# Kernel tuning notes

Hardware: AMD Instinct MI355X
Metric: run time of the kernel (lower is better)

The kernel has to match this reference:

```python
import jax, jax.numpy as jnp
import numpy as np
from jax import lax

# ---- Haar (db1) wavelet filters, matching create_wavelet_filter ----
_S2 = float(1.0 / np.sqrt(2.0))
_dec_lo = np.array([_S2, _S2], np.float32)    # pywt dec_lo reversed (symmetric)
_dec_hi = np.array([_S2, -_S2], np.float32)   # pywt dec_hi [-s,s] reversed
_rec_lo = np.array([_S2, _S2], np.float32)    # pywt rec_lo flipped (symmetric)
_rec_hi = np.array([-_S2, _S2], np.float32)   # pywt rec_hi [s,-s] flipped

def _outer(a, b):  # torch: a.unsqueeze(0) * b.unsqueeze(1) -> [i,j] = a[j]*b[i]
    return b[:, None] * a[None, :]

DEC = jnp.asarray(np.stack([_outer(_dec_lo, _dec_lo), _outer(_dec_lo, _dec_hi),
                            _outer(_dec_hi, _dec_lo), _outer(_dec_hi, _dec_hi)]))  # [4,2,2]
REC = jnp.asarray(np.stack([_outer(_rec_lo, _rec_lo), _outer(_rec_lo, _rec_hi),
                            _outer(_rec_hi, _rec_lo), _outer(_rec_hi, _rec_hi)]))  # [4,2,2]

BN_EPS = 1e-5

def mish(x):
    return x * jnp.tanh(jax.nn.softplus(x))

def silu(x):
    return x * jax.nn.sigmoid(x)

def bn(x, g, b):  # eval-mode BatchNorm2d with running_mean=0, running_var=1
    return x * (g / jnp.sqrt(1.0 + BN_EPS))[None, :, None, None] + b[None, :, None, None]

def dwconv(x, w, pad):  # depthwise conv, w: [C,1,k,k]
    return lax.conv_general_dilated(x, w, (1, 1), [(pad, pad), (pad, pad)],
                                    feature_group_count=x.shape[1],
                                    dimension_numbers=('NCHW', 'OIHW', 'NCHW'))

def dyn_dwconv(x, ew, gw):
    # DynamicConv2d (depthwise experts). ew: [E,C,1,k,k], gw: [E,C]
    gates = jax.nn.softmax(x.mean((2, 3)) @ gw.T, axis=-1)  # [B,E]
    k = ew.shape[-1]
    outs = jnp.stack([dwconv(x, ew[e], k // 2) for e in range(ew.shape[0])], 1)  # [B,E,C,H,W]
    return jnp.einsum('be,bechw->bchw', gates, outs)

def local_branch(x, ew, gw, bn1g, bn1b, pw, bn2g, bn2b):
    # DWConv2d_BN_ReLU: dynamic dwconv -> BN -> Mish -> depthwise 1x1 (per-channel scale) -> BN
    y = mish(bn(dyn_dwconv(x, ew, gw), bn1g, bn1b))
    y = y * pw[None, :, None, None]
    return bn(y, bn2g, bn2b)

def sel_scan(u, xw, dtw, dtb, Alog, Dp):
    # u: [B,L,D]; xw: [R+2N,D]; dtw: [D,R]; dtb: [D]; Alog: [D,N]; Dp: [D]
    R = dtw.shape[1]
    N = Alog.shape[1]
    xdbl = jnp.einsum('bld,ed->ble', u, xw)
    dt, Bm, Cm = xdbl[..., :R], xdbl[..., R:R + N], xdbl[..., R + N:]
    delta = jax.nn.softplus(jnp.einsum('blr,dr->bld', dt, dtw) + dtb)  # [B,L,D]
    A = -jnp.exp(Alog)                                                  # [D,N]
    a = jnp.exp(delta[..., None] * A)                                   # [B,L,D,N]
    b = delta[..., None] * Bm[:, :, None, :] * u[..., None]             # [B,L,D,N]
    def comb(c1, c2):
        a1, b1 = c1
        a2, b2 = c2
        return a1 * a2, a2 * b1 + b2
    _, h = lax.associative_scan(comb, (a, b), axis=1)                    # h_t = a_t h_{t-1} + b_t
    return jnp.einsum('bldn,bln->bld', h, Cm) + Dp * u

def ss2d(x, in_w, cw, cb, xpw, dtw, dtb, Alog, Dp, ow):
    # SS2D (d_state=1, k_group=2, channel_first): in_proj -> dwconv+silu -> 2-direction
    # selective scan -> gate with silu(z) -> out_proj.
    B, C, H, W = x.shape
    xz = jnp.einsum('oc,bchw->bohw', in_w, x)
    d = in_w.shape[0] // 2
    xi, z = xz[:, :d], xz[:, d:]
    xc = silu(dwconv(xi, cw, 1) + cb[None, :, None, None])
    u0 = xc.reshape(B, d, H * W).transpose(0, 2, 1)                       # row-major scan
    u1 = xc.transpose(0, 1, 3, 2).reshape(B, d, H * W).transpose(0, 2, 1)  # col-major scan
    y0 = sel_scan(u0, xpw[0], dtw[0], dtb[0], Alog[0], Dp[0])
    y1 = sel_scan(u1, xpw[1], dtw[1], dtb[1], Alog[1], Dp[1])
    y0 = y0.transpose(0, 2, 1).reshape(B, d, H, W)
    y1 = y1.transpose(0, 2, 1).reshape(B, d, W, H).transpose(0, 1, 3, 2)
    y = (y0 + y1) * silu(z)
    return jnp.einsum('oc,bchw->bohw', ow, y)

def mbwt(x, wav_w, wav_b, wav_scale, base_scale,
         ss_in_w, ss_conv_w, ss_conv_b, ss_xproj_w, ss_dt_w, ss_dt_b, ss_A_log, ss_D, ss_out_w):
    # MBWTConv2d, wt_levels=1, H/W even. Haar WT (2x2 stride 2) == block reshape + einsum.
    B, C, H, W = x.shape
    xr = x.reshape(B, C, H // 2, 2, W // 2, 2)
    wt = jnp.einsum('bchpwq,kpq->bckhw', xr, DEC)                  # [B,C,4,h,w]
    tag = wt.reshape(B, 4 * C, H // 2, W // 2)
    tag = dwconv(tag, wav_w, wav_w.shape[-1] // 2) + wav_b[None, :, None, None]
    tag = (tag * wav_scale).reshape(B, C, 4, H // 2, W // 2)
    # inverse Haar WT (conv_transpose 2x2 stride 2, groups=C)
    up = jnp.einsum('bckhw,kpq->bchpwq', tag, REC).reshape(B, C, H, W)
    g = ss2d(x, ss_in_w, ss_conv_w, ss_conv_b, ss_xproj_w, ss_dt_w, ss_dt_b, ss_A_log, ss_D, ss_out_w)
    return base_scale * g + up


def setup_inputs() -> dict:
    key = jax.random.key(0)
    ks = iter(jax.random.split(key, 64))
    B, DIM, H, W = 16, 256, 64, 64
    Cg = Cl = 64
    d = {'x': jax.random.normal(next(ks), (B, DIM, H, W), jnp.float32)}
    for j, k in enumerate((3, 5, 7)):
        p = f'l{j}_'
        d[p + 'ew'] = jax.random.normal(next(ks), (4, Cl, 1, k, k), jnp.float32) * 0.1
        d[p + 'gw'] = jax.random.normal(next(ks), (4, Cl), jnp.float32) * 0.1
        d[p + 'bn1g'] = jnp.ones((Cl,), jnp.float32)
        d[p + 'bn1b'] = jnp.zeros((Cl,), jnp.float32)
        d[p + 'pw'] = jax.random.normal(next(ks), (Cl,), jnp.float32) * 0.2
        d[p + 'bn2g'] = jnp.ones((Cl,), jnp.float32)
        d[p + 'bn2b'] = jnp.zeros((Cl,), jnp.float32)
    d['wav_w'] = jax.random.normal(next(ks), (4 * Cg, 1, 3, 3), jnp.float32) * 0.1
    d['wav_b'] = jnp.zeros((4 * Cg,), jnp.float32)
    d['wav_scale'] = jnp.full((1, 4 * Cg, 1, 1), 0.1, jnp.float32)
    d['base_scale'] = jnp.ones((1, Cg, 1, 1), jnp.float32)
    dm, R, N, K = Cg, 4, 1, 2  # d_inner, dt_rank, d_state, k_group
    d['ss_in_w'] = jax.random.normal(next(ks), (2 * dm, Cg), jnp.float32) * float(1 / np.sqrt(Cg))
    d['ss_conv_w'] = jax.random.normal(next(ks), (dm, 1, 3, 3), jnp.float32) * 0.1
    d['ss_conv_b'] = jnp.zeros((dm,), jnp.float32)
    d['ss_xproj_w'] = jax.random.normal(next(ks), (K, R + 2 * N, dm), jnp.float32) * float(1 / np.sqrt(dm))
    d['ss_dt_w'] = jax.random.normal(next(ks), (K, dm, R), jnp.float32) * float(1 / np.sqrt(R))
    d['ss_dt_b'] = jnp.full((K, dm), -2.0, jnp.float32)
    d['ss_A_log'] = jnp.zeros((K, dm, N), jnp.float32)
    d['ss_D'] = jnp.ones((K, dm), jnp.float32)
    d['ss_out_w'] = jax.random.normal(next(ks), (Cg, dm), jnp.float32) * float(1 / np.sqrt(dm))
    return d


def reference(x,
              l0_ew, l0_gw, l0_bn1g, l0_bn1b, l0_pw, l0_bn2g, l0_bn2b,
              l1_ew, l1_gw, l1_bn1g, l1_bn1b, l1_pw, l1_bn2g, l1_bn2b,
              l2_ew, l2_gw, l2_bn1g, l2_bn1b, l2_pw, l2_bn2g, l2_bn2b,
              wav_w, wav_b, wav_scale, base_scale,
              ss_in_w, ss_conv_w, ss_conv_b, ss_xproj_w, ss_dt_w, ss_dt_b, ss_A_log, ss_D, ss_out_w):
    Cg, Cl = 64, 64
    xg, xl, xi = x[:, :Cg], x[:, Cg:Cg + Cl], x[:, Cg + Cl:]
    yl = (local_branch(xl, l0_ew, l0_gw, l0_bn1g, l0_bn1b, l0_pw, l0_bn2g, l0_bn2b)
          + local_branch(xl, l1_ew, l1_gw, l1_bn1g, l1_bn1b, l1_pw, l1_bn2g, l1_bn2b)
          + local_branch(xl, l2_ew, l2_gw, l2_bn1g, l2_bn1b, l2_pw, l2_bn2g, l2_bn2b))
    yg = mbwt(xg, wav_w, wav_b, wav_scale, base_scale,
              ss_in_w, ss_conv_w, ss_conv_b, ss_xproj_w, ss_dt_w, ss_dt_b, ss_A_log, ss_D, ss_out_w)
    return jnp.concatenate([yg, yl, xi], axis=1)
```

## Files before the change

### kernel.cpp

```cpp
#include <hip/hip_runtime.h>
#include <math.h>

static constexpr int NB   = 16;
static constexpr int DIM  = 256;
static constexpr int CG   = 64;
static constexpr int HH   = 64;
static constexpr int WW   = 64;
static constexpr int HW   = HH * WW;

__device__ __forceinline__ float mish_fast(float x) {
    float t = __expf(fminf(x, 20.f));
    float p = __builtin_fmaf(t, t, t + t);
    return x * p * __builtin_amdgcn_rcpf(p + 2.f);
}
__device__ __forceinline__ float silu_f(float x) {
    return x * __builtin_amdgcn_rcpf(1.f + __expf(-x));
}
__device__ __forceinline__ float softplus_fast(float x) {
    return fmaxf(x, 0.f) + __logf(1.f + __expf(-fabsf(x)));
}

__global__ void k_weff_all(const float* __restrict__ mean,
                           const float* __restrict__ ew3, const float* __restrict__ gw3,
                           const float* __restrict__ g13,
                           const float* __restrict__ ew5, const float* __restrict__ gw5,
                           const float* __restrict__ g15,
                           const float* __restrict__ ew7, const float* __restrict__ gw7,
                           const float* __restrict__ g17,
                           float* __restrict__ w3o, float* __restrict__ w5o,
                           float* __restrict__ w7o) {
    int b = blockIdx.x;
    int c = threadIdx.x;
    __shared__ float m[64];
    __shared__ float g[4];
    m[c] = mean[b * 64 + c];
    __syncthreads();
    const float rs = rsqrtf(1.f + 1e-5f);

#define WEFF_SECT(GW, EW, G1, OUT, K2)                                        \
    {                                                                         \
        if (c < 4) {                                                          \
            float l = 0.f;                                                    \
            for (int cc = 0; cc < 64; ++cc) l += m[cc] * GW[c * 64 + cc];     \
            g[c] = l;                                                         \
        }                                                                     \
        __syncthreads();                                                      \
        if (c == 0) {                                                         \
            float mx = fmaxf(fmaxf(g[0], g[1]), fmaxf(g[2], g[3]));           \
            float e0 = expf(g[0] - mx), e1 = expf(g[1] - mx);                 \
            float e2 = expf(g[2] - mx), e3 = expf(g[3] - mx);                 \
            float inv = 1.f / (e0 + e1 + e2 + e3);                            \
            g[0] = e0 * inv; g[1] = e1 * inv; g[2] = e2 * inv; g[3] = e3 * inv;\
        }                                                                     \
        __syncthreads();                                                      \
        float g1s = G1[c] * rs;                                               \
        for (int kk = 0; kk < K2; ++kk) {                                     \
            float w = 0.f;                                                    \
            for (int e = 0; e < 4; ++e) w += g[e] * EW[(e * 64 + c) * K2 + kk];\
            OUT[(b * 64 + c) * K2 + kk] = w * g1s;                            \
        }                                                                     \
        __syncthreads();                                                      \
    }

    WEFF_SECT(gw3, ew3, g13, w3o, 9)
    WEFF_SECT(gw5, ew5, g15, w5o, 25)
    WEFF_SECT(gw7, ew7, g17, w7o, 49)
#undef WEFF_SECT
}

__global__ __launch_bounds__(256) void k_local(
    const float* __restrict__ x,
    const float* __restrict__ w3, const float* __restrict__ w5, const float* __restrict__ w7,
    const float* __restrict__ b1_0, const float* __restrict__ pw0,
    const float* __restrict__ g2_0, const float* __restrict__ b2_0,
    const float* __restrict__ b1_1, const float* __restrict__ pw1,
    const float* __restrict__ g2_1, const float* __restrict__ b2_1,
    const float* __restrict__ b1_2, const float* __restrict__ pw2,
    const float* __restrict__ g2_2, const float* __restrict__ b2_2,
    float* __restrict__ out) {
    int tile = blockIdx.x;
    int c = blockIdx.y, b = blockIdx.z;
    int oy = (tile >> 1) * 32, ox = (tile & 1) * 32;
    __shared__ float t[38 * 40];
    const float* xp = x + ((size_t)b * DIM + 64 + c) * HW;
    for (int i = threadIdx.x; i < 38 * 38; i += 256) {
        int r = i / 38, cc = i % 38;
        int yy = r - 3 + oy, xx = cc - 3 + ox;
        t[r * 40 + cc] = (yy >= 0 && yy < 64 && xx >= 0 && xx < 64) ? xp[yy * 64 + xx] : 0.f;
    }
    {
        int bl = tile + 4 * c + 256 * b;
        const float4* x4 = (const float4*)x;
        float4* o4 = (float4*)out;
        int base = bl * 512;
#pragma unroll
        for (int it = 0; it < 2; ++it) {
            int idx = base + it * 256 + threadIdx.x;
            int bb = idx >> 17;
            int r  = idx & 131071;
            int gi = bb * 262144 + 131072 + r;
            o4[gi] = x4[gi];
        }
    }
    const float* w3p = w3 + (b * 64 + c) * 9;
    const float* w5p = w5 + (b * 64 + c) * 25;
    const float* w7p = w7 + (b * 64 + c) * 49;
    float W3r[9], W5r[25], W7r[49];
#pragma unroll
    for (int j = 0; j < 9; ++j)  W3r[j] = w3p[j];
#pragma unroll
    for (int j = 0; j < 25; ++j) W5r[j] = w5p[j];
#pragma unroll
    for (int j = 0; j < 49; ++j) W7r[j] = w7p[j];
    __syncthreads();

    const float rs = rsqrtf(1.f + 1e-5f);
    float bb1a = b1_0[c], bb1b = b1_1[c], bb1c = b1_2[c];
    float ssa = pw0[c] * g2_0[c] * rs, ssb = pw1[c] * g2_1[c] * rs, ssc = pw2[c] * g2_2[c] * rs;
    float bb2a = b2_0[c], bb2b = b2_1[c], bb2c = b2_2[c];

    int y  = threadIdx.x >> 3;
    int x0 = (threadIdx.x & 7) * 4;

    float a3[4] = {0.f, 0.f, 0.f, 0.f};
    float a5[4] = {0.f, 0.f, 0.f, 0.f};
    float a7[4] = {0.f, 0.f, 0.f, 0.f};

#pragma unroll
    for (int dy = 0; dy < 7; ++dy) {
        const float4* rp = (const float4*)(t + (y + dy) * 40 + x0);
        float4 q0 = rp[0], q1 = rp[1], q2 = rp[2];
        float r[12] = {q0.x, q0.y, q0.z, q0.w, q1.x, q1.y, q1.z, q1.w,
                       q2.x, q2.y, q2.z, q2.w};
#pragma unroll
        for (int k = 0; k < 4; ++k)
#pragma unroll
            for (int dx = 0; dx < 7; ++dx)
                a7[k] = fmaf(r[k + dx], W7r[dy * 7 + dx], a7[k]);
        if (dy >= 1 && dy <= 5) {
            int ey = dy - 1;
#pragma unroll
            for (int k = 0; k < 4; ++k)
#pragma unroll
                for (int dx = 0; dx < 5; ++dx)
                    a5[k] = fmaf(r[k + 1 + dx], W5r[ey * 5 + dx], a5[k]);
        }
        if (dy >= 2 && dy <= 4) {
            int ey = dy - 2;
#pragma unroll
            for (int k = 0; k < 4; ++k)
#pragma unroll
                for (int dx = 0; dx < 3; ++dx)
                    a3[k] = fmaf(r[k + 2 + dx], W3r[ey * 3 + dx], a3[k]);
        }
    }

    float4 res;
    float* rr = (float*)&res;
#pragma unroll
    for (int k = 0; k < 4; ++k) {
        rr[k] = mish_fast(a3[k] + bb1a) * ssa + bb2a
              + mish_fast(a5[k] + bb1b) * ssb + bb2b
              + mish_fast(a7[k] + bb1c) * ssc + bb2c;
    }
    float* op = out + ((size_t)b * DIM + 64 + c) * HW;
    *(float4*)(op + (oy + y) * 64 + ox + x0) = res;
}

__global__ __launch_bounds__(256) void k_up(const float* __restrict__ x,
                                            const float* __restrict__ wav_w,
                                            const float* __restrict__ wav_b,
                                            const float* __restrict__ wav_scale,
                                            float* __restrict__ up,
                                            float* __restrict__ mean) {
    int c = blockIdx.x, b = blockIdx.y;
    __shared__ float xs[64 * 65];
    __shared__ float wt[4][32 * 33];
    __shared__ float red[256];
    const float* xp = x + ((size_t)b * DIM + c) * HW;
    for (int i = threadIdx.x; i < HW; i += 256) xs[(i >> 6) * 65 + (i & 63)] = xp[i];
    {
        const float* lp = x + ((size_t)b * DIM + 64 + c) * HW;
        float s = 0.f;
        for (int i = threadIdx.x; i < HW; i += 256) s += lp[i];
        red[threadIdx.x] = s;
        __syncthreads();
        for (int o = 128; o > 0; o >>= 1) {
            if (threadIdx.x < o) red[threadIdx.x] += red[threadIdx.x + o];
            __syncthreads();
        }
        if (threadIdx.x == 0) mean[b * 64 + c] = red[0] * (1.f / HW);
    }
    for (int i = threadIdx.x; i < 1024; i += 256) {
        int h = i >> 5, w = i & 31;
        float a  = xs[(2 * h) * 65 + 2 * w],     bb = xs[(2 * h) * 65 + 2 * w + 1];
        float cc = xs[(2 * h + 1) * 65 + 2 * w], dd = xs[(2 * h + 1) * 65 + 2 * w + 1];
        wt[0][h * 33 + w] = 0.5f * (a + bb + cc + dd);
        wt[1][h * 33 + w] = 0.5f * (a + bb - cc - dd);
        wt[2][h * 33 + w] = 0.5f * (a - bb + cc - dd);
        wt[3][h * 33 + w] = 0.5f * (a - bb - cc + dd);
    }
    __syncthreads();
    float wk[4][9], tb[4];
#pragma unroll
    for (int k = 0; k < 4; ++k) {
        int ch = c * 4 + k;
        float sc = wav_scale[ch];
#pragma unroll
        for (int j = 0; j < 9; ++j) wk[k][j] = wav_w[ch * 9 + j] * sc;
        tb[k] = wav_b[ch] * sc;
    }
    float* upp = up + ((size_t)b * CG + c) * HW;
    for (int i = threadIdx.x; i < 1024; i += 256) {
        int h = i >> 5, w = i & 31;
        float tg[4];
#pragma unroll
        for (int k = 0; k < 4; ++k) {
            float s = tb[k];
#pragma unroll
            for (int dy = -1; dy <= 1; ++dy) {
                int hh = h + dy;
                if (hh < 0 || hh >= 32) continue;
#pragma unroll
                for (int dx = -1; dx <= 1; ++dx) {
                    int wx = w + dx;
                    if (wx < 0 || wx >= 32) continue;
                    s = fmaf(wt[k][hh * 33 + wx], wk[k][(dy + 1) * 3 + (dx + 1)], s);
                }
            }
            tg[k] = s;
        }
        float u00 = 0.5f * (tg[0] - tg[1] - tg[2] + tg[3]);
        float u01 = 0.5f * (tg[0] - tg[1] + tg[2] - tg[3]);
        float u10 = 0.5f * (tg[0] + tg[1] - tg[2] - tg[3]);
        float u11 = 0.5f * (tg[0] + tg[1] + tg[2] + tg[3]);
        upp[(2 * h) * 64 + 2 * w]         = u00;
        upp[(2 * h) * 64 + 2 * w + 1]     = u01;
        upp[(2 * h + 1) * 64 + 2 * w]     = u10;
        upp[(2 * h + 1) * 64 + 2 * w + 1] = u11;
    }
}

__global__ __launch_bounds__(256) void k_inproj(const float* __restrict__ x,
                                                const float* __restrict__ in_w,
                                                float* __restrict__ xi,
                                                float* __restrict__ z) {
    int h0 = blockIdx.x * 2;
    int b  = blockIdx.y;
    __shared__ float xs[32 * 128];
    __shared__ float wt[32 * 128];
    int tid = threadIdx.x;

    float acc[8][8];
#pragma unroll
    for (int i = 0; i < 8; ++i)
#pragma unroll
        for (int j = 0; j < 8; ++j) acc[i][j] = 0.f;

    int o0 = (tid >> 4) * 8;
    int p0 = (tid & 15) * 8;

    for (int ko = 0; ko < 64; ko += 32) {
        if (ko) __syncthreads();
        {
            int s = tid;
#pragma unroll
            for (int it = 0; it < 4; ++it, s += 256) {
                int c = s >> 5, p4 = (s & 31) * 4;
                float4 v = *(const float4*)(x + ((size_t)b * DIM + ko + c) * HW + h0 * 64 + p4);
                *(float4*)(xs + c * 128 + p4) = v;
            }
        }
        {
            int s = tid;
#pragma unroll
            for (int it = 0; it < 4; ++it, s += 256) {
                int o = s >> 3, c0 = (s & 7) * 4;
                float4 v = *(const float4*)(in_w + o * 64 + ko + c0);
                wt[(c0 + 0) * 128 + o] = v.x;
                wt[(c0 + 1) * 128 + o] = v.y;
                wt[(c0 + 2) * 128 + o] = v.z;
                wt[(c0 + 3) * 128 + o] = v.w;
            }
        }
        __syncthreads();
#pragma unroll 4
        for (int c = 0; c < 32; ++c) {
            float xv[8], wv[8];
            *(float4*)(xv)     = *(const float4*)(xs + c * 128 + p0);
            *(float4*)(xv + 4) = *(const float4*)(xs + c * 128 + p0 + 4);
            *(float4*)(wv)     = *(const float4*)(wt + c * 128 + o0);
            *(float4*)(wv + 4) = *(const float4*)(wt + c * 128 + o0 + 4);
#pragma unroll
            for (int i = 0; i < 8; ++i)
#pragma unroll
                for (int j = 0; j < 8; ++j)
                    acc[i][j] = fmaf(wv[i], xv[j], acc[i][j]);
        }
    }

#pragma unroll
    for (int i = 0; i < 8; ++i) {
        int o = o0 + i;
        float* dst = (o < 64) ? (xi + ((size_t)b * 64 + o) * HW + h0 * 64)
                              : (z + ((size_t)b * 64 + (o - 64)) * HW + h0 * 64);
        *(float4*)(dst + p0)     = make_float4(acc[i][0], acc[i][1], acc[i][2], acc[i][3]);
        *(float4*)(dst + p0 + 4) = make_float4(acc[i][4], acc[i][5], acc[i][6], acc[i][7]);
    }
}

__global__ __launch_bounds__(256) void k_convproj(const float* __restrict__ xi,
                                                  const float* __restrict__ cw,
                                                  const float* __restrict__ cb,
                                                  const float* __restrict__ xpw,
                                                  float* __restrict__ xc,
                                                  float4* __restrict__ proj4,
                                                  float2* __restrict__ projBC) {
    int h0 = blockIdx.x * 2;
    int b  = blockIdx.y;
    int tid = threadIdx.x;

    __shared__ float xs[32 * 264];
    __shared__ float xcs[32 * 130];

    int dir = tid >> 7;
    int px  = tid & 127;
    float acc0 = 0.f, acc1 = 0.f, acc2 = 0.f, acc3 = 0.f, acc4 = 0.f, acc5 = 0.f;

    int cl_c = tid >> 3;
    int p0_c = (tid & 7) * 16;
    int row_c = p0_c >> 6;
    int wb_c  = p0_c & 63;

    for (int ch0 = 0; ch0 < 64; ch0 += 32) {
        if (ch0) __syncthreads();
        {
            int s = tid;
#pragma unroll
            for (int it = 0; it < 8; ++it, s += 256) {
                int c = s >> 6;
                int rem = s & 63;
                int r = rem >> 4, w4 = (rem & 15) * 4;
                int gh = h0 - 1 + r;
                float4 v = make_float4(0.f, 0.f, 0.f, 0.f);
                if (gh >= 0 && gh < 64)
                    v = *(const float4*)(xi + ((size_t)b * 64 + ch0 + c) * HW + gh * 64 + w4);
                float* dp = xs + c * 264 + r * 66 + 1 + w4;
                dp[0] = v.x; dp[1] = v.y; dp[2] = v.z; dp[3] = v.w;
            }
            if (tid < 128) {
                int cl = tid >> 2, r = tid & 3;
                xs[cl * 264 + r * 66 + 0]  = 0.f;
                xs[cl * 264 + r * 66 + 65] = 0.f;
            }
        }
        __syncthreads();

        {
            float wk[9];
#pragma unroll
            for (int j = 0; j < 9; ++j) wk[j] = cw[(ch0 + cl_c) * 9 + j];
            float bias = cb[ch0 + cl_c];
            float accr[16];
#pragma unroll
            for (int k = 0; k < 16; ++k) accr[k] = bias;
#pragma unroll
            for (int dy = 0; dy < 3; ++dy) {
                const float* rp = xs + cl_c * 264 + (row_c + dy) * 66 + wb_c;
                float r[18];
#pragma unroll
                for (int q = 0; q < 18; ++q) r[q] = rp[q];
#pragma unroll
                for (int k = 0; k < 16; ++k)
#pragma unroll
                    for (int dx = 0; dx < 3; ++dx)
                        accr[k] = fmaf(r[k + dx], wk[dy * 3 + dx], accr[k]);
            }
#pragma unroll
            for (int k = 0; k < 16; ++k)
                xcs[cl_c * 130 + p0_c + k] = silu_f(accr[k]);
        }
        __syncthreads();

        {
            int s = tid;
#pragma unroll
            for (int it = 0; it < 4; ++it, s += 256) {
                int c = s >> 5, pq = (s & 31) * 4;
                const float* sp = xcs + c * 130 + pq;
                *(float4*)(xc + ((size_t)b * 64 + ch0 + c) * HW + h0 * 64 + pq) =
                    make_float4(sp[0], sp[1], sp[2], sp[3]);
            }
        }
        {
            const float* wp = xpw + dir * 6 * 64 + ch0;
#pragma unroll 8
            for (int c = 0; c < 32; ++c) {
                float xv = xcs[c * 130 + px];
                acc0 = fmaf(xv, wp[0 * 64 + c], acc0);
                acc1 = fmaf(xv, wp[1 * 64 + c], acc1);
                acc2 = fmaf(xv, wp[2 * 64 + c], acc2);
                acc3 = fmaf(xv, wp[3 * 64 + c], acc3);
                acc4 = fmaf(xv, wp[4 * 64 + c], acc4);
                acc5 = fmaf(xv, wp[5 * 64 + c], acc5);
            }
        }
    }

    int h = h0 + (px >> 6), w = px & 63;
    int l = (dir == 0) ? (h * 64 + w) : (w * 64 + h);
    size_t base = ((size_t)dir * NB + b) * HW + l;
    proj4[base]  = make_float4(acc0, acc1, acc2, acc3);
    projBC[base] = make_float2(acc4, acc5);
}

__global__ __launch_bounds__(256) void k_scan2(const float* __restrict__ xc,
                                               const float4* __restrict__ proj4,
                                               const float2* __restrict__ projBC,
                                               const float* __restrict__ dt_w,
                                               const float* __restrict__ dt_b,
                                               const float* __restrict__ A_log,
                                               const float* __restrict__ Dp,
                                               const float* __restrict__ z,
                                               float* __restrict__ yz) {
    int wave = threadIdx.x >> 6;
    int lane = threadIdx.x & 63;
    int wid = blockIdx.x;
    int b = wid >> 6;
    int d = wid & 63;

    __shared__ float ut[64 * 65];
    __shared__ float al[4][1088];
    __shared__ float bl[4][1088];
    __shared__ float aggA[4], aggB[4];

    const float* uplane = xc + ((size_t)b * 64 + d) * HW;
    const float4* up4 = (const float4*)uplane;
#pragma unroll
    for (int q = 0; q < 4; ++q) {
        int s = q * 256 + threadIdx.x;
        float4 v = up4[s];
        int r = s >> 4, c0 = (s & 15) * 4;
        float* p = ut + r * 65 + c0;
        p[0] = v.x; p[1] = v.y; p[2] = v.z; p[3] = v.w;
    }
    __syncthreads();

    int ch = wave;
    float* a_my = al[wave];
    float* b_my = bl[wave];
    float y0r[16];

    {
        float4 wv = *(const float4*)(dt_w + d * 4);
        float db = dt_b[d];
        float A = -__expf(A_log[d]);
        float Dv = Dp[d];
        const float4* p4 = proj4 + (size_t)b * HW;
        const float2* pBC = projBC + (size_t)b * HW;

        float uv[16], cm[16];
#pragma unroll
        for (int j = 0; j < 16; ++j) {
            int el = j * 64 + lane;
            int e  = ch * 1024 + el;
            float4 t4 = p4[e];
            float2 t2 = pBC[e];
            float u = ut[(ch * 16 + j) * 65 + lane];
            uv[j] = u; cm[j] = t2.y;
            float pre = fmaf(t4.x, wv.x, fmaf(t4.y, wv.y,
                        fmaf(t4.z, wv.z, fmaf(t4.w, wv.w, db))));
            float delta = softplus_fast(pre);
            float aj = __expf(delta * A);
            float bj = delta * t2.x * u;
            int idx = (el >> 4) * 17 + (el & 15);
            a_my[idx] = aj;
            b_my[idx] = bj;
        }
        __builtin_amdgcn_wave_barrier();

        float a[16], bb[16];
#pragma unroll
        for (int j = 0; j < 16; ++j) {
            a[j]  = a_my[lane * 17 + j];
            bb[j] = b_my[lane * 17 + j];
        }
        float As = 1.f, Bs = 0.f;
#pragma unroll
        for (int j = 0; j < 16; ++j) { Bs = fmaf(a[j], Bs, bb[j]); As *= a[j]; }
        float Ai = As, Bi = Bs;
#pragma unroll
        for (int off = 1; off < 64; off <<= 1) {
            float ap = __shfl_up(Ai, (unsigned)off, 64);
            float bp = __shfl_up(Bi, (unsigned)off, 64);
            if (lane >= off) { Bi = fmaf(Ai, bp, Bi); Ai *= ap; }
        }
        if (lane == 63) { aggA[wave] = Ai; aggB[wave] = Bi; }
        __syncthreads();
        float carry = 0.f;
        for (int k = 0; k < wave; ++k) carry = fmaf(aggA[k], carry, aggB[k]);
        float ap1 = __shfl_up(Ai, 1, 64);
        float bp1 = __shfl_up(Bi, 1, 64);
        float h = (lane == 0) ? carry : fmaf(ap1, carry, bp1);
#pragma unroll
        for (int j = 0; j < 16; ++j) {
            h = fmaf(a[j], h, bb[j]);
            a_my[lane * 17 + j] = h;
        }
        __builtin_amdgcn_wave_barrier();
#pragma unroll
        for (int j = 0; j < 16; ++j) {
            int el = j * 64 + lane;
            float hv = a_my[(el >> 4) * 17 + (el & 15)];
            y0r[j] = fmaf(hv, cm[j], Dv * uv[j]);
        }
    }
    __syncthreads();

    {
        int pd = 64 + d;
        float4 wv = *(const float4*)(dt_w + pd * 4);
        float db = dt_b[pd];
        float A = -__expf(A_log[pd]);
        float Dv = Dp[pd];
        const float4* p4 = proj4 + ((size_t)NB + b) * HW;
        const float2* pBC = projBC + ((size_t)NB + b) * HW;

        float uv[16], cm[16];
#pragma unroll
        for (int j = 0; j < 16; ++j) {
            int el = j * 64 + lane;
            int e  = ch * 1024 + el;
            float4 t4 = p4[e];
            float2 t2 = pBC[e];
            float u = ut[lane * 65 + (ch * 16 + j)];
            uv[j] = u; cm[j] = t2.y;
            float pre = fmaf(t4.x, wv.x, fmaf(t4.y, wv.y,
                        fmaf(t4.z, wv.z, fmaf(t4.w, wv.w, db))));
            float delta = softplus_fast(pre);
            float aj = __expf(delta * A);
            float bj = delta * t2.x * u;
            int idx = (el >> 4) * 17 + (el & 15);
            a_my[idx] = aj;
            b_my[idx] = bj;
        }
        __builtin_amdgcn_wave_barrier();

        float a[16], bb[16];
#pragma unroll
        for (int j = 0; j < 16; ++j) {
            a[j]  = a_my[lane * 17 + j];
            bb[j] = b_my[lane * 17 + j];
        }
        float As = 1.f, Bs = 0.f;
#pragma unroll
        for (int j = 0; j < 16; ++j) { Bs = fmaf(a[j], Bs, bb[j]); As *= a[j]; }
        float Ai = As, Bi = Bs;
#pragma unroll
        for (int off = 1; off < 64; off <<= 1) {
            float ap = __shfl_up(Ai, (unsigned)off, 64);
            float bp = __shfl_up(Bi, (unsigned)off, 64);
            if (lane >= off) { Bi = fmaf(Ai, bp, Bi); Ai *= ap; }
        }
        if (lane == 63) { aggA[wave] = Ai; aggB[wave] = Bi; }
        __syncthreads();
        float carry = 0.f;
        for (int k = 0; k < wave; ++k) carry = fmaf(aggA[k], carry, aggB[k]);
        float ap1 = __shfl_up(Ai, 1, 64);
        float bp1 = __shfl_up(Bi, 1, 64);
        float h = (lane == 0) ? carry : fmaf(ap1, carry, bp1);
#pragma unroll
        for (int j = 0; j < 16; ++j) {
            h = fmaf(a[j], h, bb[j]);
            a_my[lane * 17 + j] = h;
        }
        __builtin_amdgcn_wave_barrier();
#pragma unroll
        for (int j = 0; j < 16; ++j) {
            int el = j * 64 + lane;
            float hv = a_my[(el >> 4) * 17 + (el & 15)];
            ut[lane * 65 + (ch * 16 + j)] = fmaf(hv, cm[j], Dv * uv[j]);
        }
    }
    __syncthreads();

    const float* zp = z + ((size_t)b * 64 + d) * HW;
    float* yp = yz + ((size_t)b * 64 + d) * HW;
#pragma unroll
    for (int j = 0; j < 16; ++j) {
        int e = ch * 1024 + j * 64 + lane;
        float y1v = ut[(ch * 16 + j) * 65 + lane];
        float zz = zp[e];
        yp[e] = (y0r[j] + y1v) * silu_f(zz);
    }
}

__global__ __launch_bounds__(256) void k_final(const float* __restrict__ yz,
                                               const float* __restrict__ ow,
                                               const float* __restrict__ base_scale,
                                               const float* __restrict__ up,
                                               float* __restrict__ out) {
    int h0 = blockIdx.x * 2;
    int b  = blockIdx.y;
    __shared__ float yv[32 * 128];
    __shared__ float wt[32 * 64];
    int tid = threadIdx.x;

    float acc[8][4];
#pragma unroll
    for (int i = 0; i < 8; ++i)
#pragma unroll
        for (int j = 0; j < 4; ++j) acc[i][j] = 0.f;

    int o0 = (tid >> 5) * 8;
    int p0 = (tid & 31) * 4;

    for (int ko = 0; ko < 64; ko += 32) {
        if (ko) __syncthreads();
        {
            int s = tid;
#pragma unroll
            for (int it = 0; it < 4; ++it, s += 256) {
                int c = s >> 5, p4 = (s & 31) * 4;
                size_t idx = ((size_t)b * 64 + ko + c) * HW + h0 * 64 + p4;
                *(float4*)(yv + c * 128 + p4) = *(const float4*)(yz + idx);
            }
        }
        {
            int s = tid;
#pragma unroll
            for (int it = 0; it < 2; ++it, s += 256) {
                int o = s >> 3, c0 = (s & 7) * 4;
                float4 v = *(const float4*)(ow + o * 64 + ko + c0);
                wt[(c0 + 0) * 64 + o] = v.x;
                wt[(c0 + 1) * 64 + o] = v.y;
                wt[(c0 + 2) * 64 + o] = v.z;
                wt[(c0 + 3) * 64 + o] = v.w;
            }
        }
        __syncthreads();
#pragma unroll 4
        for (int c = 0; c < 32; ++c) {
            float wv[8], xv[4];
            *(float4*)(wv)     = *(const float4*)(wt + c * 64 + o0);
            *(float4*)(wv + 4) = *(const float4*)(wt + c * 64 + o0 + 4);
            *(float4*)(xv)     = *(const float4*)(yv + c * 128 + p0);
#pragma unroll
            for (int i = 0; i < 8; ++i)
#pragma unroll
                for (int j = 0; j < 4; ++j)
                    acc[i][j] = fmaf(wv[i], xv[j], acc[i][j]);
        }
    }

#pragma unroll
    for (int i = 0; i < 8; ++i) {
        int o = o0 + i;
        float bs = base_scale[o];
        float4 u = *(const float4*)(up + ((size_t)b * 64 + o) * HW + h0 * 64 + p0);
        float4 r = make_float4(fmaf(bs, acc[i][0], u.x),
                               fmaf(bs, acc[i][1], u.y),
                               fmaf(bs, acc[i][2], u.z),
                               fmaf(bs, acc[i][3], u.w));
        *(float4*)(out + ((size_t)b * DIM + o) * HW + h0 * 64 + p0) = r;
    }
}

extern "C" void kernel_launch(void* const* d_in, const int* in_sizes, int n_in,
                              void* d_out, int out_size, void* d_ws, size_t ws_size,
                              hipStream_t stream) {
    (void)in_sizes; (void)n_in; (void)out_size; (void)ws_size;
    const float* x = (const float*)d_in[0];
    float* out = (float*)d_out;
    float* ws = (float*)d_ws;

    const size_t IMG = (size_t)NB * 64 * HW;
    float* buf_xi   = ws;
    float* buf_z    = ws + IMG;
    float* buf_xc   = ws + 2 * IMG;
    float* buf_up   = ws + 3 * IMG;
    float* buf_p4   = ws + 4 * IMG;
    float* buf_pBC  = buf_p4 + (size_t)4 * 2 * NB * HW;
    float* buf_mean = buf_pBC + (size_t)2 * 2 * NB * HW;
    float* buf_w3   = buf_mean + 1024;
    float* buf_w5   = buf_w3 + 16 * 64 * 9;
    float* buf_w7   = buf_w5 + 16 * 64 * 25;

    k_up<<<dim3(64, 16), 256, 0, stream>>>(x, (const float*)d_in[22],
        (const float*)d_in[23], (const float*)d_in[24], buf_up, buf_mean);

    k_weff_all<<<16, 64, 0, stream>>>(buf_mean,
        (const float*)d_in[1],  (const float*)d_in[2],  (const float*)d_in[3],
        (const float*)d_in[8],  (const float*)d_in[9],  (const float*)d_in[10],
        (const float*)d_in[15], (const float*)d_in[16], (const float*)d_in[17],
        buf_w3, buf_w5, buf_w7);
    k_local<<<dim3(4, 64, 16), 256, 0, stream>>>(x, buf_w3, buf_w5, buf_w7,
        (const float*)d_in[4],  (const float*)d_in[5],  (const float*)d_in[6],  (const float*)d_in[7],
        (const float*)d_in[11], (const float*)d_in[12], (const float*)d_in[13], (const float*)d_in[14],
        (const float*)d_in[18], (const float*)d_in[19], (const float*)d_in[20], (const float*)d_in[21],
        out);

    k_inproj<<<dim3(32, 16), 256, 0, stream>>>(x, (const float*)d_in[26], buf_xi, buf_z);
    k_convproj<<<dim3(32, 16), 256, 0, stream>>>(buf_xi, (const float*)d_in[27],
        (const float*)d_in[28], (const float*)d_in[29],
        buf_xc, (float4*)buf_p4, (float2*)buf_pBC);
    k_scan2<<<1024, 256, 0, stream>>>(buf_xc, (const float4*)buf_p4, (const float2*)buf_pBC,
        (const float*)d_in[30], (const float*)d_in[31],
        (const float*)d_in[32], (const float*)d_in[33],
        buf_z, buf_xi );
    k_final<<<dim3(32, 16), 256, 0, stream>>>(buf_xi,
        (const float*)d_in[34], (const float*)d_in[25], buf_up, out);
}
```

Before: 138.5 us.

## Merge independent kernels into horizontally fused stage launches

Seven launches become four by branching on block index. Independent work shares one grid: wavelet upsample with the in-projection, conv-projection with the expert-weight mixing, and the local branch with the final out-projection. This cuts launch gaps and lets the small, under-filled kernels overlap with the larger ones. In exchange, shared memory is sized for the largest branch and register pressure follows the heaviest branch, which can lower occupancy for all blocks.

```diff
diff --git a/kernel.cpp b/kernel.cpp
--- a/kernel.cpp
+++ b/kernel.cpp
@@ -20,398 +20,300 @@
     return fmaxf(x, 0.f) + __logf(1.f + __expf(-fabsf(x)));
 }
 
-__global__ void k_weff_all(const float* __restrict__ mean,
-                           const float* __restrict__ ew3, const float* __restrict__ gw3,
-                           const float* __restrict__ g13,
-                           const float* __restrict__ ew5, const float* __restrict__ gw5,
-                           const float* __restrict__ g15,
-                           const float* __restrict__ ew7, const float* __restrict__ gw7,
-                           const float* __restrict__ g17,
-                           float* __restrict__ w3o, float* __restrict__ w5o,
-                           float* __restrict__ w7o) {
-    int b = blockIdx.x;
-    int c = threadIdx.x;
-    __shared__ float m[64];
-    __shared__ float g[4];
-    m[c] = mean[b * 64 + c];
-    __syncthreads();
-    const float rs = rsqrtf(1.f + 1e-5f);
-
-#define WEFF_SECT(GW, EW, G1, OUT, K2)                                        \
-    {                                                                         \
-        if (c < 4) {                                                          \
-            float l = 0.f;                                                    \
-            for (int cc = 0; cc < 64; ++cc) l += m[cc] * GW[c * 64 + cc];     \
-            g[c] = l;                                                         \
-        }                                                                     \
-        __syncthreads();                                                      \
-        if (c == 0) {                                                         \
-            float mx = fmaxf(fmaxf(g[0], g[1]), fmaxf(g[2], g[3]));           \
-            float e0 = expf(g[0] - mx), e1 = expf(g[1] - mx);                 \
-            float e2 = expf(g[2] - mx), e3 = expf(g[3] - mx);                 \
-            float inv = 1.f / (e0 + e1 + e2 + e3);                            \
-            g[0] = e0 * inv; g[1] = e1 * inv; g[2] = e2 * inv; g[3] = e3 * inv;\
-        }                                                                     \
-        __syncthreads();                                                      \
-        float g1s = G1[c] * rs;                                               \
-        for (int kk = 0; kk < K2; ++kk) {                                     \
-            float w = 0.f;                                                    \
-            for (int e = 0; e < 4; ++e) w += g[e] * EW[(e * 64 + c) * K2 + kk];\
-            OUT[(b * 64 + c) * K2 + kk] = w * g1s;                            \
-        }                                                                     \
-        __syncthreads();                                                      \
-    }
-
-    WEFF_SECT(gw3, ew3, g13, w3o, 9)
-    WEFF_SECT(gw5, ew5, g15, w5o, 25)
-    WEFF_SECT(gw7, ew7, g17, w7o, 49)
-#undef WEFF_SECT
-}
-
-__global__ __launch_bounds__(256) void k_local(
+__global__ __launch_bounds__(256) void k_stage1(
     const float* __restrict__ x,
-    const float* __restrict__ w3, const float* __restrict__ w5, const float* __restrict__ w7,
-    const float* __restrict__ b1_0, const float* __restrict__ pw0,
-    const float* __restrict__ g2_0, const float* __restrict__ b2_0,
-    const float* __restrict__ b1_1, const float* __restrict__ pw1,
-    const float* __restrict__ g2_1, const float* __restrict__ b2_1,
-    const float* __restrict__ b1_2, const float* __restrict__ pw2,
-    const float* __restrict__ g2_2, const float* __restrict__ b2_2,
-    float* __restrict__ out) {
-    int tile = blockIdx.x;
-    int c = blockIdx.y, b = blockIdx.z;
-    int oy = (tile >> 1) * 32, ox = (tile & 1) * 32;
-    __shared__ float t[38 * 40];
-    const float* xp = x + ((size_t)b * DIM + 64 + c) * HW;
-    for (int i = threadIdx.x; i < 38 * 38; i += 256) {
-        int r = i / 38, cc = i % 38;
-        int yy = r - 3 + oy, xx = cc - 3 + ox;
-        t[r * 40 + cc] = (yy >= 0 && yy < 64 && xx >= 0 && xx < 64) ? xp[yy * 64 + xx] : 0.f;
-    }
-    {
-        int bl = tile + 4 * c + 256 * b;
-        const float4* x4 = (const float4*)x;
-        float4* o4 = (float4*)out;
-        int base = bl * 512;
-#pragma unroll
-        for (int it = 0; it < 2; ++it) {
-            int idx = base + it * 256 + threadIdx.x;
-            int bb = idx >> 17;
-            int r  = idx & 131071;
-            int gi = bb * 262144 + 131072 + r;
-            o4[gi] = x4[gi];
-        }
-    }
-    const float* w3p = w3 + (b * 64 + c) * 9;
-    const float* w5p = w5 + (b * 64 + c) * 25;
-    const float* w7p = w7 + (b * 64 + c) * 49;
-    float W3r[9], W5r[25], W7r[49];
-#pragma unroll
-    for (int j = 0; j < 9; ++j)  W3r[j] = w3p[j];
-#pragma unroll
-    for (int j = 0; j < 25; ++j) W5r[j] = w5p[j];
-#pragma unroll
-    for (int j = 0; j < 49; ++j) W7r[j] = w7p[j];
-    __syncthreads();
-
-    const float rs = rsqrtf(1.f + 1e-5f);
-    float bb1a = b1_0[c], bb1b = b1_1[c], bb1c = b1_2[c];
-    float ssa = pw0[c] * g2_0[c] * rs, ssb = pw1[c] * g2_1[c] * rs, ssc = pw2[c] * g2_2[c] * rs;
-    float bb2a = b2_0[c], bb2b = b2_1[c], bb2c = b2_2[c];
-
-    int y  = threadIdx.x >> 3;
-    int x0 = (threadIdx.x & 7) * 4;
-
-    float a3[4] = {0.f, 0.f, 0.f, 0.f};
-    float a5[4] = {0.f, 0.f, 0.f, 0.f};
-    float a7[4] = {0.f, 0.f, 0.f, 0.f};
-
-#pragma unroll
-    for (int dy = 0; dy < 7; ++dy) {
-        const float4* rp = (const float4*)(t + (y + dy) * 40 + x0);
-        float4 q0 = rp[0], q1 = rp[1], q2 = rp[2];
-        float r[12] = {q0.x, q0.y, q0.z, q0.w, q1.x, q1.y, q1.z, q1.w,
-                       q2.x, q2.y, q2.z, q2.w};
-#pragma unroll
-        for (int k = 0; k < 4; ++k)
-#pragma unroll
-            for (int dx = 0; dx < 7; ++dx)
-                a7[k] = fmaf(r[k + dx], W7r[dy * 7 + dx], a7[k]);
-        if (dy >= 1 && dy <= 5) {
-            int ey = dy - 1;
-#pragma unroll
-            for (int k = 0; k < 4; ++k)
-#pragma unroll
-                for (int dx = 0; dx < 5; ++dx)
-                    a5[k] = fmaf(r[k + 1 + dx], W5r[ey * 5 + dx], a5[k]);
-        }
-        if (dy >= 2 && dy <= 4) {
-            int ey = dy - 2;
-#pragma unroll
-            for (int k = 0; k < 4; ++k)
-#pragma unroll
-                for (int dx = 0; dx < 3; ++dx)
-                    a3[k] = fmaf(r[k + 2 + dx], W3r[ey * 3 + dx], a3[k]);
-        }
-    }
-
-    float4 res;
-    float* rr = (float*)&res;
-#pragma unroll
-    for (int k = 0; k < 4; ++k) {
-        rr[k] = mish_fast(a3[k] + bb1a) * ssa + bb2a
-              + mish_fast(a5[k] + bb1b) * ssb + bb2b
-              + mish_fast(a7[k] + bb1c) * ssc + bb2c;
-    }
-    float* op = out + ((size_t)b * DIM + 64 + c) * HW;
-    *(float4*)(op + (oy + y) * 64 + ox + x0) = res;
-}
-
-__global__ __launch_bounds__(256) void k_up(const float* __restrict__ x,
-                                            const float* __restrict__ wav_w,
-                                            const float* __restrict__ wav_b,
-                                            const float* __restrict__ wav_scale,
-                                            float* __restrict__ up,
-                                            float* __restrict__ mean) {
-    int c = blockIdx.x, b = blockIdx.y;
-    __shared__ float xs[64 * 65];
-    __shared__ float wt[4][32 * 33];
-    __shared__ float red[256];
-    const float* xp = x + ((size_t)b * DIM + c) * HW;
-    for (int i = threadIdx.x; i < HW; i += 256) xs[(i >> 6) * 65 + (i & 63)] = xp[i];
-    {
-        const float* lp = x + ((size_t)b * DIM + 64 + c) * HW;
-        float s = 0.f;
-        for (int i = threadIdx.x; i < HW; i += 256) s += lp[i];
-        red[threadIdx.x] = s;
+    const float* __restrict__ wav_w, const float* __restrict__ wav_b,
+    const float* __restrict__ wav_scale,
+    float* __restrict__ up, float* __restrict__ mean,
+    const float* __restrict__ in_w,
+    float* __restrict__ xi, float* __restrict__ z) {
+    __shared__ float smem[8640];
+    int bid = blockIdx.x;
+    int tid = threadIdx.x;
+
+    if (bid < 1024) {
+        int c = bid & 63, b = bid >> 6;
+        float* xs  = smem;
+        float* wtb = smem + 4160;
+        float* red = smem + 8384;
+        const float* xp = x + ((size_t)b * DIM + c) * HW;
+        for (int i = tid; i < HW; i += 256) xs[(i >> 6) * 65 + (i & 63)] = xp[i];
+        {
+            const float* lp = x + ((size_t)b * DIM + 64 + c) * HW;
+            float s = 0.f;
+            for (int i = tid; i < HW; i += 256) s += lp[i];
+            red[tid] = s;
+            __syncthreads();
+            for (int o = 128; o > 0; o >>= 1) {
+                if (tid < o) red[tid] += red[tid + o];
+                __syncthreads();
+            }
+            if (tid == 0) mean[b * 64 + c] = red[0] * (1.f / HW);
+        }
+        for (int i = tid; i < 1024; i += 256) {
+            int h = i >> 5, w = i & 31;
+            float a  = xs[(2 * h) * 65 + 2 * w],     bb = xs[(2 * h) * 65 + 2 * w + 1];
+            float cc = xs[(2 * h + 1) * 65 + 2 * w], dd = xs[(2 * h + 1) * 65 + 2 * w + 1];
+            wtb[0 * 1056 + h * 33 + w] = 0.5f * (a + bb + cc + dd);
+            wtb[1 * 1056 + h * 33 + w] = 0.5f * (a + bb - cc - dd);
+            wtb[2 * 1056 + h * 33 + w] = 0.5f * (a - bb + cc - dd);
+            wtb[3 * 1056 + h * 33 + w] = 0.5f * (a - bb - cc + dd);
+        }
         __syncthreads();
-        for (int o = 128; o > 0; o >>= 1) {
-            if (threadIdx.x < o) red[threadIdx.x] += red[threadIdx.x + o];
+        float wk[4][9], tb[4];
+#pragma unroll
+        for (int k = 0; k < 4; ++k) {
+            int ch = c * 4 + k;
+            float sc = wav_scale[ch];
+#pragma unroll
+            for (int j = 0; j < 9; ++j) wk[k][j] = wav_w[ch * 9 + j] * sc;
+            tb[k] = wav_b[ch] * sc;
+        }
+        float* upp = up + ((size_t)b * CG + c) * HW;
+        for (int i = tid; i < 1024; i += 256) {
+            int h = i >> 5, w = i & 31;
+            float tg[4];
+#pragma unroll
+            for (int k = 0; k < 4; ++k) {
+                float s = tb[k];
+#pragma unroll
+                for (int dy = -1; dy <= 1; ++dy) {
+                    int hh = h + dy;
+                    if (hh < 0 || hh >= 32) continue;
+#pragma unroll
+                    for (int dx = -1; dx <= 1; ++dx) {
+                        int wx = w + dx;
+                        if (wx < 0 || wx >= 32) continue;
+                        s = fmaf(wtb[k * 1056 + hh * 33 + wx], wk[k][(dy + 1) * 3 + (dx + 1)], s);
+                    }
+                }
+                tg[k] = s;
+            }
+            float u00 = 0.5f * (tg[0] - tg[1] - tg[2] + tg[3]);
+            float u01 = 0.5f * (tg[0] - tg[1] + tg[2] - tg[3]);
+            float u10 = 0.5f * (tg[0] + tg[1] - tg[2] - tg[3]);
+            float u11 = 0.5f * (tg[0] + tg[1] + tg[2] + tg[3]);
+            upp[(2 * h) * 64 + 2 * w]         = u00;
+            upp[(2 * h) * 64 + 2 * w + 1]     = u01;
+            upp[(2 * h + 1) * 64 + 2 * w]     = u10;
+            upp[(2 * h + 1) * 64 + 2 * w + 1] = u11;
+        }
+    } else {
+        int id2 = bid - 1024;
+        int h0 = (id2 & 31) * 2;
+        int b  = id2 >> 5;
+        float* xs = smem;
+        float* wt = smem + 4096;
+
+        float acc[8][8];
+#pragma unroll
+        for (int i = 0; i < 8; ++i)
+#pragma unroll
+            for (int j = 0; j < 8; ++j) acc[i][j] = 0.f;
+
+        int o0 = (tid >> 4) * 8;
+        int p0 = (tid & 15) * 8;
+
+        for (int ko = 0; ko < 64; ko += 32) {
+            if (ko) __syncthreads();
+            {
+                int s = tid;
+#pragma unroll
+                for (int it = 0; it < 4; ++it, s += 256) {
+                    int c = s >> 5, p4 = (s & 31) * 4;
+                    float4 v = *(const float4*)(x + ((size_t)b * DIM + ko + c) * HW + h0 * 64 + p4);
+                    *(float4*)(xs + c * 128 + p4) = v;
+                }
+            }
+            {
+                int s = tid;
+#pragma unroll
+                for (int it = 0; it < 4; ++it, s += 256) {
+                    int o = s >> 3, c0 = (s & 7) * 4;
+                    float4 v = *(const float4*)(in_w + o * 64 + ko + c0);
+                    wt[(c0 + 0) * 128 + o] = v.x;
+                    wt[(c0 + 1) * 128 + o] = v.y;
+                    wt[(c0 + 2) * 128 + o] = v.z;
+                    wt[(c0 + 3) * 128 + o] = v.w;
+                }
+            }
             __syncthreads();
-        }
-        if (threadIdx.x == 0) mean[b * 64 + c] = red[0] * (1.f / HW);
-    }
-    for (int i = threadIdx.x; i < 1024; i += 256) {
-        int h = i >> 5, w = i & 31;
-        float a  = xs[(2 * h) * 65 + 2 * w],     bb = xs[(2 * h) * 65 + 2 * w + 1];
-        float cc = xs[(2 * h + 1) * 65 + 2 * w], dd = xs[(2 * h + 1) * 65 + 2 * w + 1];
-        wt[0][h * 33 + w] = 0.5f * (a + bb + cc + dd);
-        wt[1][h * 33 + w] = 0.5f * (a + bb - cc - dd);
-        wt[2][h * 33 + w] = 0.5f * (a - bb + cc - dd);
-        wt[3][h * 33 + w] = 0.5f * (a - bb - cc + dd);
-    }
-    __syncthreads();
-    float wk[4][9], tb[4];
-#pragma unroll
-    for (int k = 0; k < 4; ++k) {
-        int ch = c * 4 + k;
-        float sc = wav_scale[ch];
-#pragma unroll
-        for (int j = 0; j < 9; ++j) wk[k][j] = wav_w[ch * 9 + j] * sc;
-        tb[k] = wav_b[ch] * sc;
-    }
-    float* upp = up + ((size_t)b * CG + c) * HW;
-    for (int i = threadIdx.x; i < 1024; i += 256) {
-        int h = i >> 5, w = i & 31;
-        float tg[4];
-#pragma unroll
-        for (int k = 0; k < 4; ++k) {
-            float s = tb[k];
-#pragma unroll
-            for (int dy = -1; dy <= 1; ++dy) {
-                int hh = h + dy;
-                if (hh < 0 || hh >= 32) continue;
-#pragma unroll
-                for (int dx = -1; dx <= 1; ++dx) {
-                    int wx = w + dx;
-                    if (wx < 0 || wx >= 32) continue;
-                    s = fmaf(wt[k][hh * 33 + wx], wk[k][(dy + 1) * 3 + (dx + 1)], s);
-                }
-            }
-            tg[k] = s;
-        }
-        float u00 = 0.5f * (tg[0] - tg[1] - tg[2] + tg[3]);
-        float u01 = 0.5f * (tg[0] - tg[1] + tg[2] - tg[3]);
-        float u10 = 0.5f * (tg[0] + tg[1] - tg[2] - tg[3]);
-        float u11 = 0.5f * (tg[0] + tg[1] + tg[2] + tg[3]);
-        upp[(2 * h) * 64 + 2 * w]         = u00;
-        upp[(2 * h) * 64 + 2 * w + 1]     = u01;
-        upp[(2 * h + 1) * 64 + 2 * w]     = u10;
-        upp[(2 * h + 1) * 64 + 2 * w + 1] = u11;
+#pragma unroll 4
+            for (int c = 0; c < 32; ++c) {
+                float xv[8], wv[8];
+                *(float4*)(xv)     = *(const float4*)(xs + c * 128 + p0);
+                *(float4*)(xv + 4) = *(const float4*)(xs + c * 128 + p0 + 4);
+                *(float4*)(wv)     = *(const float4*)(wt + c * 128 + o0);
+                *(float4*)(wv + 4) = *(const float4*)(wt + c * 128 + o0 + 4);
+#pragma unroll
+                for (int i = 0; i < 8; ++i)
+#pragma unroll
+                    for (int j = 0; j < 8; ++j)
+                        acc[i][j] = fmaf(wv[i], xv[j], acc[i][j]);
+            }
+        }
+
+#pragma unroll
+        for (int i = 0; i < 8; ++i) {
+            int o = o0 + i;
+            float* dst = (o < 64) ? (xi + ((size_t)b * 64 + o) * HW + h0 * 64)
+                                  : (z + ((size_t)b * 64 + (o - 64)) * HW + h0 * 64);
+            *(float4*)(dst + p0)     = make_float4(acc[i][0], acc[i][1], acc[i][2], acc[i][3]);
+            *(float4*)(dst + p0 + 4) = make_float4(acc[i][4], acc[i][5], acc[i][6], acc[i][7]);
+        }
     }
 }
 
-__global__ __launch_bounds__(256) void k_inproj(const float* __restrict__ x,
-                                                const float* __restrict__ in_w,
-                                                float* __restrict__ xi,
-                                                float* __restrict__ z) {
-    int h0 = blockIdx.x * 2;
-    int b  = blockIdx.y;
-    __shared__ float xs[32 * 128];
-    __shared__ float wt[32 * 128];
+__global__ __launch_bounds__(256) void k_stage2(
+    const float* __restrict__ xi,
+    const float* __restrict__ cw, const float* __restrict__ cb,
+    const float* __restrict__ xpw,
+    float* __restrict__ xc, float4* __restrict__ proj4, float2* __restrict__ projBC,
+    const float* __restrict__ mean,
+    const float* __restrict__ ew3, const float* __restrict__ gw3, const float* __restrict__ g13,
+    const float* __restrict__ ew5, const float* __restrict__ gw5, const float* __restrict__ g15,
+    const float* __restrict__ ew7, const float* __restrict__ gw7, const float* __restrict__ g17,
+    float* __restrict__ w3o, float* __restrict__ w5o, float* __restrict__ w7o) {
+    __shared__ float smem[12608];
+    int bid = blockIdx.x;
     int tid = threadIdx.x;
 
-    float acc[8][8];
-#pragma unroll
-    for (int i = 0; i < 8; ++i)
-#pragma unroll
-        for (int j = 0; j < 8; ++j) acc[i][j] = 0.f;
-
-    int o0 = (tid >> 4) * 8;
-    int p0 = (tid & 15) * 8;
-
-    for (int ko = 0; ko < 64; ko += 32) {
-        if (ko) __syncthreads();
-        {
-            int s = tid;
-#pragma unroll
-            for (int it = 0; it < 4; ++it, s += 256) {
-                int c = s >> 5, p4 = (s & 31) * 4;
-                float4 v = *(const float4*)(x + ((size_t)b * DIM + ko + c) * HW + h0 * 64 + p4);
-                *(float4*)(xs + c * 128 + p4) = v;
-            }
-        }
-        {
-            int s = tid;
-#pragma unroll
-            for (int it = 0; it < 4; ++it, s += 256) {
-                int o = s >> 3, c0 = (s & 7) * 4;
-                float4 v = *(const float4*)(in_w + o * 64 + ko + c0);
-                wt[(c0 + 0) * 128 + o] = v.x;
-                wt[(c0 + 1) * 128 + o] = v.y;
-                wt[(c0 + 2) * 128 + o] = v.z;
-                wt[(c0 + 3) * 128 + o] = v.w;
-            }
-        }
+    if (bid < 512) {
+        int h0 = (bid & 31) * 2;
+        int b  = bid >> 5;
+        float* xs  = smem;
+        float* xcs = smem + 8448;
+
+        int dir = tid >> 7;
+        int px  = tid & 127;
+        float acc0 = 0.f, acc1 = 0.f, acc2 = 0.f, acc3 = 0.f, acc4 = 0.f, acc5 = 0.f;
+
+        int cl_c = tid >> 3;
+        int p0_c = (tid & 7) * 16;
+        int row_c = p0_c >> 6;
+        int wb_c  = p0_c & 63;
+
+        for (int ch0 = 0; ch0 < 64; ch0 += 32) {
+            if (ch0) __syncthreads();
+            {
+                int s = tid;
+#pragma unroll
+                for (int it = 0; it < 8; ++it, s += 256) {
+                    int c = s >> 6;
+                    int rem = s & 63;
+                    int r = rem >> 4, w4 = (rem & 15) * 4;
+                    int gh = h0 - 1 + r;
+                    float4 v = make_float4(0.f, 0.f, 0.f, 0.f);
+                    if (gh >= 0 && gh < 64)
+                        v = *(const float4*)(xi + ((size_t)b * 64 + ch0 + c) * HW + gh * 64 + w4);
+                    float* dp = xs + c * 264 + r * 66 + 1 + w4;
+                    dp[0] = v.x; dp[1] = v.y; dp[2] = v.z; dp[3] = v.w;
+                }
+                if (tid < 128) {
+                    int cl = tid >> 2, r = tid & 3;
+                    xs[cl * 264 + r * 66 + 0]  = 0.f;
+                    xs[cl * 264 + r * 66 + 65] = 0.f;
+                }
+            }
+            __syncthreads();
+
+            {
+                float wk[9];
+#pragma unroll
+                for (int j = 0; j < 9; ++j) wk[j] = cw[(ch0 + cl_c) * 9 + j];
+                float bias = cb[ch0 + cl_c];
+                float accr[16];
+#pragma unroll
+                for (int k = 0; k < 16; ++k) accr[k] = bias;
+#pragma unroll
+                for (int dy = 0; dy < 3; ++dy) {
+                    const float* rp = xs + cl_c * 264 + (row_c + dy) * 66 + wb_c;
+                    float r[18];
+#pragma unroll
+                    for (int q = 0; q < 18; ++q) r[q] = rp[q];
+#pragma unroll
+                    for (int k = 0; k < 16; ++k)
+#pragma unroll
+                        for (int dx = 0; dx < 3; ++dx)
+                            accr[k] = fmaf(r[k + dx], wk[dy * 3 + dx], accr[k]);
+                }
+#pragma unroll
+                for (int k = 0; k < 16; ++k)
+                    xcs[cl_c * 130 + p0_c + k] = silu_f(accr[k]);
+            }
+            __syncthreads();
+
+            {
+                int s = tid;
+#pragma unroll
+                for (int it = 0; it < 4; ++it, s += 256) {
+                    int c = s >> 5, pq = (s & 31) * 4;
+                    const float* sp = xcs + c * 130 + pq;
+                    *(float4*)(xc + ((size_t)b * 64 + ch0 + c) * HW + h0 * 64 + pq) =
+                        make_float4(sp[0], sp[1], sp[2], sp[3]);
+                }
+            }
+            {
+                const float* wp = xpw + dir * 6 * 64 + ch0;
+#pragma unroll 8
+                for (int c = 0; c < 32; ++c) {
+                    float xv = xcs[c * 130 + px];
+                    acc0 = fmaf(xv, wp[0 * 64 + c], acc0);
+                    acc1 = fmaf(xv, wp[1 * 64 + c], acc1);
+                    acc2 = fmaf(xv, wp[2 * 64 + c], acc2);
+                    acc3 = fmaf(xv, wp[3 * 64 + c], acc3);
+                    acc4 = fmaf(xv, wp[4 * 64 + c], acc4);
+                    acc5 = fmaf(xv, wp[5 * 64 + c], acc5);
+                }
+            }
+        }
+
+        int h = h0 + (px >> 6), w = px & 63;
+        int l = (dir == 0) ? (h * 64 + w) : (w * 64 + h);
+        size_t base = ((size_t)dir * NB + b) * HW + l;
+        proj4[base]  = make_float4(acc0, acc1, acc2, acc3);
+        projBC[base] = make_float2(acc4, acc5);
+    } else {
+        int b = bid - 512;
+        int c = tid;
+        float* m = smem;
+        float* g = smem + 64;
+        if (c < 64) m[c] = mean[b * 64 + c];
         __syncthreads();
-#pragma unroll 4
-        for (int c = 0; c < 32; ++c) {
-            float xv[8], wv[8];
-            *(float4*)(xv)     = *(const float4*)(xs + c * 128 + p0);
-            *(float4*)(xv + 4) = *(const float4*)(xs + c * 128 + p0 + 4);
-            *(float4*)(wv)     = *(const float4*)(wt + c * 128 + o0);
-            *(float4*)(wv + 4) = *(const float4*)(wt + c * 128 + o0 + 4);
-#pragma unroll
-            for (int i = 0; i < 8; ++i)
-#pragma unroll
-                for (int j = 0; j < 8; ++j)
-                    acc[i][j] = fmaf(wv[i], xv[j], acc[i][j]);
-        }
+        const float rs = rsqrtf(1.f + 1e-5f);
+
+#define WEFF_SECT(GW, EW, G1, OUT, K2)                                        \
+        {                                                                     \
+            if (c < 4) {                                                      \
+                float l = 0.f;                                                \
+                for (int cc = 0; cc < 64; ++cc) l += m[cc] * GW[c * 64 + cc]; \
+                g[c] = l;                                                     \
+            }                                                                 \
+            __syncthreads();                                                  \
+            if (c == 0) {                                                     \
+                float mx = fmaxf(fmaxf(g[0], g[1]), fmaxf(g[2], g[3]));       \
+                float e0 = expf(g[0] - mx), e1 = expf(g[1] - mx);             \
+                float e2 = expf(g[2] - mx), e3 = expf(g[3] - mx);             \
+                float inv = 1.f / (e0 + e1 + e2 + e3);                        \
+                g[0] = e0 * inv; g[1] = e1 * inv; g[2] = e2 * inv; g[3] = e3 * inv; \
+            }                                                                 \
+            __syncthreads();                                                  \
+            if (c < 64) {                                                     \
+                float g1s = G1[c] * rs;                                       \
+                for (int kk = 0; kk < K2; ++kk) {                             \
+                    float w = 0.f;                                            \
+                    for (int e = 0; e < 4; ++e) w += g[e] * EW[(e * 64 + c) * K2 + kk]; \
+                    OUT[(b * 64 + c) * K2 + kk] = w * g1s;                    \
+                }                                                             \
+            }                                                                 \
+            __syncthreads();                                                  \
+        }
+
+        WEFF_SECT(gw3, ew3, g13, w3o, 9)
+        WEFF_SECT(gw5, ew5, g15, w5o, 25)
+        WEFF_SECT(gw7, ew7, g17, w7o, 49)
+#undef WEFF_SECT
     }
-
-#pragma unroll
-    for (int i = 0; i < 8; ++i) {
-        int o = o0 + i;
-        float* dst = (o < 64) ? (xi + ((size_t)b * 64 + o) * HW + h0 * 64)
-                              : (z + ((size_t)b * 64 + (o - 64)) * HW + h0 * 64);
-        *(float4*)(dst + p0)     = make_float4(acc[i][0], acc[i][1], acc[i][2], acc[i][3]);
-        *(float4*)(dst + p0 + 4) = make_float4(acc[i][4], acc[i][5], acc[i][6], acc[i][7]);
-    }
-}
-
-__global__ __launch_bounds__(256) void k_convproj(const float* __restrict__ xi,
-                                                  const float* __restrict__ cw,
-                                                  const float* __restrict__ cb,
-                                                  const float* __restrict__ xpw,
-                                                  float* __restrict__ xc,
-                                                  float4* __restrict__ proj4,
-                                                  float2* __restrict__ projBC) {
-    int h0 = blockIdx.x * 2;
-    int b  = blockIdx.y;
-    int tid = threadIdx.x;
-
-    __shared__ float xs[32 * 264];
-    __shared__ float xcs[32 * 130];
-
-    int dir = tid >> 7;
-    int px  = tid & 127;
-    float acc0 = 0.f, acc1 = 0.f, acc2 = 0.f, acc3 = 0.f, acc4 = 0.f, acc5 = 0.f;
-
-    int cl_c = tid >> 3;
-    int p0_c = (tid & 7) * 16;
-    int row_c = p0_c >> 6;
-    int wb_c  = p0_c & 63;
-
-    for (int ch0 = 0; ch0 < 64; ch0 += 32) {
-        if (ch0) __syncthreads();
-        {
-            int s = tid;
-#pragma unroll
-            for (int it = 0; it < 8; ++it, s += 256) {
-                int c = s >> 6;
-                int rem = s & 63;
-                int r = rem >> 4, w4 = (rem & 15) * 4;
-                int gh = h0 - 1 + r;
-                float4 v = make_float4(0.f, 0.f, 0.f, 0.f);
-                if (gh >= 0 && gh < 64)
-                    v = *(const float4*)(xi + ((size_t)b * 64 + ch0 + c) * HW + gh * 64 + w4);
-                float* dp = xs + c * 264 + r * 66 + 1 + w4;
-                dp[0] = v.x; dp[1] = v.y; dp[2] = v.z; dp[3] = v.w;
-            }
-            if (tid < 128) {
-                int cl = tid >> 2, r = tid & 3;
-                xs[cl * 264 + r * 66 + 0]  = 0.f;
-                xs[cl * 264 + r * 66 + 65] = 0.f;
-            }
-        }
-        __syncthreads();
-
-        {
-            float wk[9];
-#pragma unroll
-            for (int j = 0; j < 9; ++j) wk[j] = cw[(ch0 + cl_c) * 9 + j];
-            float bias = cb[ch0 + cl_c];
-            float accr[16];
-#pragma unroll
-            for (int k = 0; k < 16; ++k) accr[k] = bias;
-#pragma unroll
-            for (int dy = 0; dy < 3; ++dy) {
-                const float* rp = xs + cl_c * 264 + (row_c + dy) * 66 + wb_c;
-                float r[18];
-#pragma unroll
-                for (int q = 0; q < 18; ++q) r[q] = rp[q];
-#pragma unroll
-                for (int k = 0; k < 16; ++k)
-#pragma unroll
-                    for (int dx = 0; dx < 3; ++dx)
-                        accr[k] = fmaf(r[k + dx], wk[dy * 3 + dx], accr[k]);
-            }
-#pragma unroll
-            for (int k = 0; k < 16; ++k)
-                xcs[cl_c * 130 + p0_c + k] = silu_f(accr[k]);
-        }
-        __syncthreads();
-
-        {
-            int s = tid;
-#pragma unroll
-            for (int it = 0; it < 4; ++it, s += 256) {
-                int c = s >> 5, pq = (s & 31) * 4;
-                const float* sp = xcs + c * 130 + pq;
-                *(float4*)(xc + ((size_t)b * 64 + ch0 + c) * HW + h0 * 64 + pq) =
-                    make_float4(sp[0], sp[1], sp[2], sp[3]);
-            }
-        }
-        {
-            const float* wp = xpw + dir * 6 * 64 + ch0;
-#pragma unroll 8
-            for (int c = 0; c < 32; ++c) {
-                float xv = xcs[c * 130 + px];
-                acc0 = fmaf(xv, wp[0 * 64 + c], acc0);
-                acc1 = fmaf(xv, wp[1 * 64 + c], acc1);
-                acc2 = fmaf(xv, wp[2 * 64 + c], acc2);
-                acc3 = fmaf(xv, wp[3 * 64 + c], acc3);
-                acc4 = fmaf(xv, wp[4 * 64 + c], acc4);
-                acc5 = fmaf(xv, wp[5 * 64 + c], acc5);
-            }
-        }
-    }
-
-    int h = h0 + (px >> 6), w = px & 63;
-    int l = (dir == 0) ? (h * 64 + w) : (w * 64 + h);
-    size_t base = ((size_t)dir * NB + b) * HW + l;
-    proj4[base]  = make_float4(acc0, acc1, acc2, acc3);
-    projBC[base] = make_float2(acc4, acc5);
 }
 
 __global__ __launch_bounds__(256) void k_scan2(const float* __restrict__ xc,
@@ -595,74 +497,175 @@
     }
 }
 
-__global__ __launch_bounds__(256) void k_final(const float* __restrict__ yz,
-                                               const float* __restrict__ ow,
-                                               const float* __restrict__ base_scale,
-                                               const float* __restrict__ up,
-                                               float* __restrict__ out) {
-    int h0 = blockIdx.x * 2;
-    int b  = blockIdx.y;
-    __shared__ float yv[32 * 128];
-    __shared__ float wt[32 * 64];
+__global__ __launch_bounds__(256) void k_stage4(
+    const float* __restrict__ x,
+    const float* __restrict__ w3, const float* __restrict__ w5, const float* __restrict__ w7,
+    const float* __restrict__ b1_0, const float* __restrict__ pw0,
+    const float* __restrict__ g2_0, const float* __restrict__ b2_0,
+    const float* __restrict__ b1_1, const float* __restrict__ pw1,
+    const float* __restrict__ g2_1, const float* __restrict__ b2_1,
+    const float* __restrict__ b1_2, const float* __restrict__ pw2,
+    const float* __restrict__ g2_2, const float* __restrict__ b2_2,
+    const float* __restrict__ yz, const float* __restrict__ ow,
+    const float* __restrict__ base_scale, const float* __restrict__ up,
+    float* __restrict__ out) {
+    __shared__ float smem[6144];
+    int bid = blockIdx.x;
     int tid = threadIdx.x;
 
-    float acc[8][4];
-#pragma unroll
-    for (int i = 0; i < 8; ++i)
-#pragma unroll
-        for (int j = 0; j < 4; ++j) acc[i][j] = 0.f;
-
-    int o0 = (tid >> 5) * 8;
-    int p0 = (tid & 31) * 4;
-
-    for (int ko = 0; ko < 64; ko += 32) {
-        if (ko) __syncthreads();
+    if (bid < 4096) {
+        int tile = bid & 3;
+        int c = (bid >> 2) & 63;
+        int b = bid >> 8;
+        int oy = (tile >> 1) * 32, ox = (tile & 1) * 32;
+        float* t = smem;
+        const float* xp = x + ((size_t)b * DIM + 64 + c) * HW;
+        for (int i = tid; i < 38 * 38; i += 256) {
+            int r = i / 38, cc = i % 38;
+            int yy = r - 3 + oy, xx = cc - 3 + ox;
+            t[r * 40 + cc] = (yy >= 0 && yy < 64 && xx >= 0 && xx < 64) ? xp[yy * 64 + xx] : 0.f;
+        }
         {
-            int s = tid;
-#pragma unroll
-            for (int it = 0; it < 4; ++it, s += 256) {
-                int c = s >> 5, p4 = (s & 31) * 4;
-                size_t idx = ((size_t)b * 64 + ko + c) * HW + h0 * 64 + p4;
-                *(float4*)(yv + c * 128 + p4) = *(const float4*)(yz + idx);
-            }
-        }
-        {
-            int s = tid;
-#pragma unroll
-            for (int it = 0; it < 2; ++it, s += 256) {
-                int o = s >> 3, c0 = (s & 7) * 4;
-                float4 v = *(const float4*)(ow + o * 64 + ko + c0);
-                wt[(c0 + 0) * 64 + o] = v.x;
-                wt[(c0 + 1) * 64 + o] = v.y;
-                wt[(c0 + 2) * 64 + o] = v.z;
-                wt[(c0 + 3) * 64 + o] = v.w;
-            }
-        }
+            const float4* x4 = (const float4*)x;
+            float4* o4 = (float4*)out;
+            int base = bid * 512;
+#pragma unroll
+            for (int it = 0; it < 2; ++it) {
+                int idx = base + it * 256 + tid;
+                int bb = idx >> 17;
+                int r  = idx & 131071;
+                int gi = bb * 262144 + 131072 + r;
+                o4[gi] = x4[gi];
+            }
+        }
+        const float* w3p = w3 + (b * 64 + c) * 9;
+        const float* w5p = w5 + (b * 64 + c) * 25;
+        const float* w7p = w7 + (b * 64 + c) * 49;
+        float W3r[9], W5r[25], W7r[49];
+#pragma unroll
+        for (int j = 0; j < 9; ++j)  W3r[j] = w3p[j];
+#pragma unroll
+        for (int j = 0; j < 25; ++j) W5r[j] = w5p[j];
+#pragma unroll
+        for (int j = 0; j < 49; ++j) W7r[j] = w7p[j];
         __syncthreads();
+
+        const float rs = rsqrtf(1.f + 1e-5f);
+        float bb1a = b1_0[c], bb1b = b1_1[c], bb1c = b1_2[c];
+        float ssa = pw0[c] * g2_0[c] * rs, ssb = pw1[c] * g2_1[c] * rs, ssc = pw2[c] * g2_2[c] * rs;
+        float bb2a = b2_0[c], bb2b = b2_1[c], bb2c = b2_2[c];
+
+        int y  = tid >> 3;
+        int x0 = (tid & 7) * 4;
+
+        float a3[4] = {0.f, 0.f, 0.f, 0.f};
+        float a5[4] = {0.f, 0.f, 0.f, 0.f};
+        float a7[4] = {0.f, 0.f, 0.f, 0.f};
+
+#pragma unroll
+        for (int dy = 0; dy < 7; ++dy) {
+            const float4* rp = (const float4*)(t + (y + dy) * 40 + x0);
+            float4 q0 = rp[0], q1 = rp[1], q2 = rp[2];
+            float r[12] = {q0.x, q0.y, q0.z, q0.w, q1.x, q1.y, q1.z, q1.w,
+                           q2.x, q2.y, q2.z, q2.w};
+#pragma unroll
+            for (int k = 0; k < 4; ++k)
+#pragma unroll
+                for (int dx = 0; dx < 7; ++dx)
+                    a7[k] = fmaf(r[k + dx], W7r[dy * 7 + dx], a7[k]);
+            if (dy >= 1 && dy <= 5) {
+                int ey = dy - 1;
+#pragma unroll
+                for (int k = 0; k < 4; ++k)
+#pragma unroll
+                    for (int dx = 0; dx < 5; ++dx)
+                        a5[k] = fmaf(r[k + 1 + dx], W5r[ey * 5 + dx], a5[k]);
+            }
+            if (dy >= 2 && dy <= 4) {
+                int ey = dy - 2;
+#pragma unroll
+                for (int k = 0; k < 4; ++k)
+#pragma unroll
+                    for (int dx = 0; dx < 3; ++dx)
+                        a3[k] = fmaf(r[k + 2 + dx], W3r[ey * 3 + dx], a3[k]);
+            }
+        }
+
+        float4 res;
+        float* rr = (float*)&res;
+#pragma unroll
+        for (int k = 0; k < 4; ++k) {
+            rr[k] = mish_fast(a3[k] + bb1a) * ssa + bb2a
+                  + mish_fast(a5[k] + bb1b) * ssb + bb2b
+                  + mish_fast(a7[k] + bb1c) * ssc + bb2c;
+        }
+        float* op = out + ((size_t)b * DIM + 64 + c) * HW;
+        *(float4*)(op + (oy + y) * 64 + ox + x0) = res;
+    } else {
+        int id2 = bid - 4096;
+        int h0 = (id2 & 31) * 2;
+        int b  = id2 >> 5;
+        float* yv = smem;
+        float* wt = smem + 4096;
+
+        float acc[8][4];
+#pragma unroll
+        for (int i = 0; i < 8; ++i)
+#pragma unroll
+            for (int j = 0; j < 4; ++j) acc[i][j] = 0.f;
+
+        int o0 = (tid >> 5) * 8;
+        int p0 = (tid & 31) * 4;
+
+        for (int ko = 0; ko < 64; ko += 32) {
+            if (ko) __syncthreads();
+            {
+                int s = tid;
+#pragma unroll
+                for (int it = 0; it < 4; ++it, s += 256) {
+                    int c = s >> 5, p4 = (s & 31) * 4;
+                    size_t idx = ((size_t)b * 64 + ko + c) * HW + h0 * 64 + p4;
+                    *(float4*)(yv + c * 128 + p4) = *(const float4*)(yz + idx);
+                }
+            }
+            {
+                int s = tid;
+#pragma unroll
+                for (int it = 0; it < 2; ++it, s += 256) {
+                    int o = s >> 3, c0 = (s & 7) * 4;
+                    float4 v = *(const float4*)(ow + o * 64 + ko + c0);
+                    wt[(c0 + 0) * 64 + o] = v.x;
+                    wt[(c0 + 1) * 64 + o] = v.y;
+                    wt[(c0 + 2) * 64 + o] = v.z;
+                    wt[(c0 + 3) * 64 + o] = v.w;
+                }
+            }
+            __syncthreads();
 #pragma unroll 4
-        for (int c = 0; c < 32; ++c) {
-            float wv[8], xv[4];
-            *(float4*)(wv)     = *(const float4*)(wt + c * 64 + o0);
-            *(float4*)(wv + 4) = *(const float4*)(wt + c * 64 + o0 + 4);
-            *(float4*)(xv)     = *(const float4*)(yv + c * 128 + p0);
-#pragma unroll
-            for (int i = 0; i < 8; ++i)
-#pragma unroll
-                for (int j = 0; j < 4; ++j)
-                    acc[i][j] = fmaf(wv[i], xv[j], acc[i][j]);
-        }
-    }
-
-#pragma unroll
-    for (int i = 0; i < 8; ++i) {
-        int o = o0 + i;
-        float bs = base_scale[o];
-        float4 u = *(const float4*)(up + ((size_t)b * 64 + o) * HW + h0 * 64 + p0);
-        float4 r = make_float4(fmaf(bs, acc[i][0], u.x),
-                               fmaf(bs, acc[i][1], u.y),
-                               fmaf(bs, acc[i][2], u.z),
-                               fmaf(bs, acc[i][3], u.w));
-        *(float4*)(out + ((size_t)b * DIM + o) * HW + h0 * 64 + p0) = r;
+            for (int c = 0; c < 32; ++c) {
+                float wv[8], xv[4];
+                *(float4*)(wv)     = *(const float4*)(wt + c * 64 + o0);
+                *(float4*)(wv + 4) = *(const float4*)(wt + c * 64 + o0 + 4);
+                *(float4*)(xv)     = *(const float4*)(yv + c * 128 + p0);
+#pragma unroll
+                for (int i = 0; i < 8; ++i)
+#pragma unroll
+                    for (int j = 0; j < 4; ++j)
+                        acc[i][j] = fmaf(wv[i], xv[j], acc[i][j]);
+            }
+        }
+
+#pragma unroll
+        for (int i = 0; i < 8; ++i) {
+            int o = o0 + i;
+            float bs = base_scale[o];
+            float4 u = *(const float4*)(up + ((size_t)b * 64 + o) * HW + h0 * 64 + p0);
+            float4 r = make_float4(fmaf(bs, acc[i][0], u.x),
+                                   fmaf(bs, acc[i][1], u.y),
+                                   fmaf(bs, acc[i][2], u.z),
+                                   fmaf(bs, acc[i][3], u.w));
+            *(float4*)(out + ((size_t)b * DIM + o) * HW + h0 * 64 + p0) = r;
+        }
     }
 }
 
@@ -686,28 +689,28 @@
     float* buf_w5   = buf_w3 + 16 * 64 * 9;
     float* buf_w7   = buf_w5 + 16 * 64 * 25;
 
-    k_up<<<dim3(64, 16), 256, 0, stream>>>(x, (const float*)d_in[22],
-        (const float*)d_in[23], (const float*)d_in[24], buf_up, buf_mean);
-
-    k_weff_all<<<16, 64, 0, stream>>>(buf_mean,
+    k_stage1<<<1536, 256, 0, stream>>>(x,
+        (const float*)d_in[22], (const float*)d_in[23], (const float*)d_in[24],
+        buf_up, buf_mean,
+        (const float*)d_in[26], buf_xi, buf_z);
+
+    k_stage2<<<528, 256, 0, stream>>>(buf_xi,
+        (const float*)d_in[27], (const float*)d_in[28], (const float*)d_in[29],
+        buf_xc, (float4*)buf_p4, (float2*)buf_pBC,
+        buf_mean,
         (const float*)d_in[1],  (const float*)d_in[2],  (const float*)d_in[3],
         (const float*)d_in[8],  (const float*)d_in[9],  (const float*)d_in[10],
         (const float*)d_in[15], (const float*)d_in[16], (const float*)d_in[17],
         buf_w3, buf_w5, buf_w7);
-    k_local<<<dim3(4, 64, 16), 256, 0, stream>>>(x, buf_w3, buf_w5, buf_w7,
+
+    k_scan2<<<1024, 256, 0, stream>>>(buf_xc, (const float4*)buf_p4, (const float2*)buf_pBC,
+        (const float*)d_in[30], (const float*)d_in[31],
+        (const float*)d_in[32], (const float*)d_in[33],
+        buf_z, buf_xi);
+
+    k_stage4<<<4608, 256, 0, stream>>>(x, buf_w3, buf_w5, buf_w7,
         (const float*)d_in[4],  (const float*)d_in[5],  (const float*)d_in[6],  (const float*)d_in[7],
         (const float*)d_in[11], (const float*)d_in[12], (const float*)d_in[13], (const float*)d_in[14],
         (const float*)d_in[18], (const float*)d_in[19], (const float*)d_in[20], (const float*)d_in[21],
-        out);
-
-    k_inproj<<<dim3(32, 16), 256, 0, stream>>>(x, (const float*)d_in[26], buf_xi, buf_z);
-    k_convproj<<<dim3(32, 16), 256, 0, stream>>>(buf_xi, (const float*)d_in[27],
-        (const float*)d_in[28], (const float*)d_in[29],
-        buf_xc, (float4*)buf_p4, (float2*)buf_pBC);
-    k_scan2<<<1024, 256, 0, stream>>>(buf_xc, (const float4*)buf_p4, (const float2*)buf_pBC,
-        (const float*)d_in[30], (const float*)d_in[31],
-        (const float*)d_in[32], (const float*)d_in[33],
-        buf_z, buf_xi );
-    k_final<<<dim3(32, 16), 256, 0, stream>>>(buf_xi,
-        (const float*)d_in[34], (const float*)d_in[25], buf_up, out);
+        buf_xi, (const float*)d_in[34], (const float*)d_in[25], buf_up, out);
 }
```

After: 126.4 us. 8.7% less time.
